# Performance work log

Measured on AMD Instinct MI355X. Metric: run time of the kernel, lower is better.

Reference implementation:

```python
import jax, jax.numpy as jnp
import numpy as np

N_VERTS = 200000
NNZ = 1600000
C_IN = 128
C_OUT = 128


def setup_inputs() -> dict:
    key = jax.random.key(0)
    k1, k2, k3, k4, k5, k6 = jax.random.split(key, 6)
    x = jax.random.normal(k1, (N_VERTS, C_IN), dtype=jnp.float32)
    rows = jax.random.randint(k2, (NNZ,), 0, N_VERTS, dtype=jnp.int64)
    cols = jax.random.randint(k3, (NNZ,), 0, N_VERTS, dtype=jnp.int64)
    vals = jax.random.normal(k4, (NNZ,), dtype=jnp.float32)
    W = jax.random.normal(k5, (C_OUT, C_IN), dtype=jnp.float32) * (1.0 / np.sqrt(C_IN))
    b = jax.random.normal(k6, (C_OUT,), dtype=jnp.float32) * 0.01
    return {"x": x, "rows": rows, "cols": cols, "vals": vals, "W": W, "b": b}


def reference(x, rows, cols, vals, W, b):
    # SpMM: out[r] += vals[e] * x[cols[e]]  (F = 2I - L in COO form)
    n = x.shape[0]
    agg = jax.ops.segment_sum(vals[:, None] * x[cols], rows, num_segments=n)  # [N, C_in]
    # Dense Linear projection: agg @ W^T + b
    return agg @ W.T + b  # [N, C_out]
```

## Files before the change

### kernel.cpp

```cpp
#include <hip/hip_runtime.h>

#define NV 200000
#define NE 1600000
#define CD 128
#define NBUCK 3125
#define NBLK 64
#define CHUNK 25600

#define Y_OFF      0UL
#define WB_OFF     51200000UL
#define CNT_OFF    51232768UL
#define TOT_OFF    52032768UL
#define START_OFF  52045312UL
#define SCAT_OFF   52058112UL
#define ROWOFF_OFF 64858112UL
#define SCAT2_OFF  65658368UL

typedef short  short8 __attribute__((ext_vector_type(8)));
typedef float  f32x4  __attribute__((ext_vector_type(4)));

__device__ __forceinline__ short bf16of(float f) {
    __bf16 h = (__bf16)f;
    return __builtin_bit_cast(short, h);
}

__global__ __launch_bounds__(256) void k_cvtW(const float* __restrict__ W,
                                              unsigned short* __restrict__ Wb) {
    int i = blockIdx.x * 256 + threadIdx.x;
    float4 wv = reinterpret_cast<const float4*>(W)[i];
    ushort4 o;
    o.x = (unsigned short)bf16of(wv.x);
    o.y = (unsigned short)bf16of(wv.y);
    o.z = (unsigned short)bf16of(wv.z);
    o.w = (unsigned short)bf16of(wv.w);
    reinterpret_cast<ushort4*>(Wb)[i] = o;
}

#define GEMM_BLOCKS 512
#define GEMM_WAVES (GEMM_BLOCKS * 4)
#define NTILES (NV / 16)

__global__ __launch_bounds__(256, 2) void gemm_mfma(const float* __restrict__ x,
                                                    const unsigned short* __restrict__ Wb,
                                                    unsigned short* __restrict__ y) {
    __shared__ __align__(16) short Wlds[2048 * 8];

    const int t = threadIdx.x;
    const int lane = t & 63;
    const int w = t >> 6;
    const int g = lane >> 4;

    {
        const uint4* Wg = reinterpret_cast<const uint4*>(Wb);
        uint4* L = reinterpret_cast<uint4*>(Wlds);
#pragma unroll
        for (int i = 0; i < 8; ++i) {
            int c = t + i * 256;
            int l = c & 63;
            int ks = (c >> 6) & 3;
            int tl = c >> 8;
            int row = 16 * tl + (l & 15);
            L[c] = Wg[row * 16 + ks * 4 + (l >> 4)];
        }
    }
    __syncthreads();

    short8 A[8][4];
    {
        const short8* L8 = reinterpret_cast<const short8*>(Wlds);
#pragma unroll
        for (int t8 = 0; t8 < 8; ++t8)
#pragma unroll
            for (int ks = 0; ks < 4; ++ks)
                A[t8][ks] = L8[(t8 * 4 + ks) * 64 + lane];
    }

    const int wgid = blockIdx.x * 4 + w;
    char* yb = reinterpret_cast<char*>(y);

    for (int tile = wgid; tile < NTILES; tile += GEMM_WAVES) {
        const int v0 = tile * 16;
        const int row = v0 + (lane & 15);
        const float4* xr = reinterpret_cast<const float4*>(x + (size_t)row * CD);

        float4 xf[8];
#pragma unroll
        for (int ks = 0; ks < 4; ++ks) {
            xf[2 * ks]     = xr[8 * ks + 2 * g];
            xf[2 * ks + 1] = xr[8 * ks + 2 * g + 1];
        }

        f32x4 acc[8];
#pragma unroll
        for (int t8 = 0; t8 < 8; ++t8) acc[t8] = (f32x4){0.f, 0.f, 0.f, 0.f};

#pragma unroll
        for (int ks = 0; ks < 4; ++ks) {
            short8 B;
            const float* f = reinterpret_cast<const float*>(&xf[2 * ks]);
#pragma unroll
            for (int j = 0; j < 8; ++j) B[j] = bf16of(f[j]);
#pragma unroll
            for (int t8 = 0; t8 < 8; ++t8)
                acc[t8] = __builtin_amdgcn_mfma_f32_16x16x32_bf16(A[t8][ks], B, acc[t8], 0, 0, 0);
        }

        const size_t rb = (size_t)(v0 + (lane & 15)) * 256;
#pragma unroll
        for (int t8 = 0; t8 < 8; ++t8) {
            ushort4 o;
            o.x = (unsigned short)bf16of(acc[t8][0]);
            o.y = (unsigned short)bf16of(acc[t8][1]);
            o.z = (unsigned short)bf16of(acc[t8][2]);
            o.w = (unsigned short)bf16of(acc[t8][3]);
            *reinterpret_cast<ushort4*>(yb + rb + t8 * 32 + g * 8) = o;
        }
    }
}

__global__ __launch_bounds__(1024) void pc(const int* __restrict__ rows,
                                           int* __restrict__ cnt) {
    __shared__ int hist[NBUCK];
    const int t = threadIdx.x;
    for (int i = t; i < NBUCK; i += 1024) hist[i] = 0;
    __syncthreads();
    const int e0 = blockIdx.x * CHUNK;
    const int e1 = min(NE, e0 + CHUNK);
    for (int e = e0 + t; e < e1; e += 1024)
        atomicAdd(&hist[rows[e] >> 6], 1);
    __syncthreads();
    for (int i = t; i < NBUCK; i += 1024)
        cnt[(size_t)blockIdx.x * NBUCK + i] = hist[i];
}

__global__ __launch_bounds__(256) void ps(int* __restrict__ cnt,
                                          int* __restrict__ tot) {
    int g = blockIdx.x * 256 + threadIdx.x;
    if (g >= NBUCK) return;
    int running = 0;
    for (int blk = 0; blk < NBLK; ++blk) {
        int idx = blk * NBUCK + g;
        int c = cnt[idx];
        cnt[idx] = running;
        running += c;
    }
    tot[g] = running;
}

__global__ __launch_bounds__(1024) void pt(const int* __restrict__ tot,
                                           int* __restrict__ start) {
    __shared__ int s[1024];
    const int t = threadIdx.x;
    if (t == 0) start[NBUCK] = NE;
    int carry = 0;
    for (int c = 0; c < 4; ++c) {
        int idx = c * 1024 + t;
        int v = (idx < NBUCK) ? tot[idx] : 0;
        s[t] = v;
        __syncthreads();
        for (int d = 1; d < 1024; d <<= 1) {
            int add = (t >= d) ? s[t - d] : 0;
            __syncthreads();
            s[t] += add;
            __syncthreads();
        }
        if (idx < NBUCK) start[idx] = carry + s[t] - v;
        carry += s[1023];
        __syncthreads();
    }
}

__global__ __launch_bounds__(1024) void px(const int* __restrict__ rows,
                                           const int* __restrict__ cols,
                                           const float* __restrict__ vals,
                                           const int* __restrict__ cnt,
                                           const int* __restrict__ start,
                                           int2* __restrict__ scat) {
    __shared__ int cur[NBUCK];
    const int t = threadIdx.x;
    for (int i = t; i < NBUCK; i += 1024)
        cur[i] = start[i] + cnt[(size_t)blockIdx.x * NBUCK + i];
    __syncthreads();
    const int e0 = blockIdx.x * CHUNK;
    const int e1 = min(NE, e0 + CHUNK);
    for (int e = e0 + t; e < e1; e += 1024) {
        int r = rows[e];
        int pos = atomicAdd(&cur[r >> 6], 1);
        scat[pos] = make_int2(cols[e] | ((r & 63) << 18), __float_as_int(vals[e]));
    }
}

__global__ __launch_bounds__(256) void k_sort(const int* __restrict__ start,
                                              const int2* __restrict__ scat,
                                              int2* __restrict__ scat2,
                                              int* __restrict__ rowoff) {
    __shared__ int rcnt[64], rinc[64], cur[64];
    const int t = threadIdx.x;
    const int b = blockIdx.x;
    const int s0 = start[b], s1 = start[b + 1];

    if (t < 64) rcnt[t] = 0;
    __syncthreads();
    for (int e = s0 + t; e < s1; e += 256)
        atomicAdd(&rcnt[(scat[e].x >> 18) & 63], 1);
    __syncthreads();
    if (t < 64) rinc[t] = rcnt[t];
    __syncthreads();
    for (int d = 1; d < 64; d <<= 1) {
        int add = 0;
        if (t < 64 && t >= d) add = rinc[t - d];
        __syncthreads();
        if (t < 64) rinc[t] += add;
        __syncthreads();
    }
    if (t < 64) {
        int excl = rinc[t] - rcnt[t];
        cur[t] = excl;
        rowoff[b * 64 + t] = s0 + excl;
    }
    if (b == NBUCK - 1 && t == 0) rowoff[NV] = NE;
    __syncthreads();
    for (int e = s0 + t; e < s1; e += 256) {
        int2 p = scat[e];
        int lr = (p.x >> 18) & 63;
        int pos = s0 + atomicAdd(&cur[lr], 1);
        scat2[pos] = p;
    }
}

#define BFLO(u) __uint_as_float((u) << 16)
#define BFHI(u) __uint_as_float((u) & 0xffff0000u)

__global__ __launch_bounds__(256) void k_gather(const int* __restrict__ rowoff,
                                                const int2* __restrict__ scat2,
                                                const unsigned* __restrict__ y,
                                                const float* __restrict__ b,
                                                float* __restrict__ out) {
    const int wid = threadIdx.x >> 6;
    const int lane = threadIdx.x & 63;
    const int half = lane >> 5;
    const int sl = lane & 31;
    const int row = blockIdx.x * 4 + wid;

    const int s0 = rowoff[row];
    const int n = rowoff[row + 1] - s0;
    const int nh = (n - half + 1) >> 1;

    float4 acc = half ? make_float4(0.f, 0.f, 0.f, 0.f)
                      : reinterpret_cast<const float4*>(b)[sl];
    const uint2* y2 = reinterpret_cast<const uint2*>(y);

    int k = 0;
    int e = s0 + half;
    for (; k + 4 <= nh; k += 4, e += 8) {
        int2 p0 = scat2[e];
        int2 p1 = scat2[e + 2];
        int2 p2 = scat2[e + 4];
        int2 p3 = scat2[e + 6];
        uint2 u0 = y2[(size_t)(p0.x & 0x3ffff) * 32 + sl];
        uint2 u1 = y2[(size_t)(p1.x & 0x3ffff) * 32 + sl];
        uint2 u2 = y2[(size_t)(p2.x & 0x3ffff) * 32 + sl];
        uint2 u3 = y2[(size_t)(p3.x & 0x3ffff) * 32 + sl];
        float v0 = __int_as_float(p0.y), v1 = __int_as_float(p1.y);
        float v2 = __int_as_float(p2.y), v3 = __int_as_float(p3.y);
        acc.x += (v0 * BFLO(u0.x) + v1 * BFLO(u1.x)) + (v2 * BFLO(u2.x) + v3 * BFLO(u3.x));
        acc.y += (v0 * BFHI(u0.x) + v1 * BFHI(u1.x)) + (v2 * BFHI(u2.x) + v3 * BFHI(u3.x));
        acc.z += (v0 * BFLO(u0.y) + v1 * BFLO(u1.y)) + (v2 * BFLO(u2.y) + v3 * BFLO(u3.y));
        acc.w += (v0 * BFHI(u0.y) + v1 * BFHI(u1.y)) + (v2 * BFHI(u2.y) + v3 * BFHI(u3.y));
    }
    for (; k < nh; ++k, e += 2) {
        int2 p = scat2[e];
        uint2 u = y2[(size_t)(p.x & 0x3ffff) * 32 + sl];
        float v = __int_as_float(p.y);
        acc.x += v * BFLO(u.x);
        acc.y += v * BFHI(u.x);
        acc.z += v * BFLO(u.y);
        acc.w += v * BFHI(u.y);
    }

    acc.x += __shfl_xor(acc.x, 32);
    acc.y += __shfl_xor(acc.y, 32);
    acc.z += __shfl_xor(acc.z, 32);
    acc.w += __shfl_xor(acc.w, 32);

    if (half == 0) {
        f32x4 st = {acc.x, acc.y, acc.z, acc.w};
        __builtin_nontemporal_store(st, (f32x4*)(out + (size_t)row * CD + sl * 4));
    }
}

extern "C" void kernel_launch(void* const* d_in, const int* in_sizes, int n_in,
                              void* d_out, int out_size, void* d_ws, size_t ws_size,
                              hipStream_t stream) {
    const float* x    = (const float*)d_in[0];
    const int*   rows = (const int*)d_in[1];
    const int*   cols = (const int*)d_in[2];
    const float* vals = (const float*)d_in[3];
    const float* Wm   = (const float*)d_in[4];
    const float* b    = (const float*)d_in[5];
    float* out = (float*)d_out;

    char* ws = (char*)d_ws;
    unsigned short* y  = (unsigned short*)(ws + Y_OFF);
    unsigned short* Wb = (unsigned short*)(ws + WB_OFF);
    int* cnt           = (int*)(ws + CNT_OFF);
    int* tot           = (int*)(ws + TOT_OFF);
    int* start         = (int*)(ws + START_OFF);
    int2* scat         = (int2*)(ws + SCAT_OFF);
    int* rowoff        = (int*)(ws + ROWOFF_OFF);
    int2* scat2        = (int2*)(ws + SCAT2_OFF);

    k_cvtW<<<16, 256, 0, stream>>>(Wm, Wb);
    gemm_mfma<<<GEMM_BLOCKS, 256, 0, stream>>>(x, Wb, y);
    pc<<<NBLK, 1024, 0, stream>>>(rows, cnt);
    ps<<<(NBUCK + 255) / 256, 256, 0, stream>>>(cnt, tot);
    pt<<<1, 1024, 0, stream>>>(tot, start);
    px<<<NBLK, 1024, 0, stream>>>(rows, cols, vals, cnt, start, scat);
    k_sort<<<NBUCK, 256, 0, stream>>>(start, scat, scat2, rowoff);
    k_gather<<<NV / 4, 256, 0, stream>>>(rowoff, scat2, (const unsigned*)y, b, out);
}
```

Measured before the change: 193.7 us.

## Fuse W conversion and row histogram into GEMM launch; widen gather loads

Removes the separate W-to-bf16 kernel by converting W to bf16 (round-to-nearest-even) inline while filling LDS in each GEMM block. It also merges the row-bucket histogram into the same launch as 64 extra blocks, so histogramming runs alongside the GEMM. The gather kernel now splits each wave into four 16-lane groups that each load full 16-byte bf16 rows, then reduces with two shuffles, replacing the two 32-lane halves doing 8-byte loads. This saves two launches and issues fewer, wider loads, at the cost of redundant W conversion in every GEMM block and histogram blocks running at 256 threads instead of 1024.

After: 184.1 us. 5.0% less time.

```diff
diff --git a/kernel.cpp b/kernel.cpp
--- a/kernel.cpp
+++ b/kernel.cpp
@@ -8,7 +8,6 @@
 #define CHUNK 25600
 
 #define Y_OFF      0UL
-#define WB_OFF     51200000UL
 #define CNT_OFF    51232768UL
 #define TOT_OFF    52032768UL
 #define START_OFF  52045312UL
@@ -19,39 +18,54 @@
 typedef short  short8 __attribute__((ext_vector_type(8)));
 typedef float  f32x4  __attribute__((ext_vector_type(4)));
 
+__device__ __forceinline__ unsigned bf16pair(float a, float b) {
+    unsigned ua = __float_as_uint(a);
+    unsigned ub = __float_as_uint(b);
+    ua += 0x7fffu + ((ua >> 16) & 1u);
+    ub += 0x7fffu + ((ub >> 16) & 1u);
+    return (ua >> 16) | (ub & 0xffff0000u);
+}
+
 __device__ __forceinline__ short bf16of(float f) {
     __bf16 h = (__bf16)f;
     return __builtin_bit_cast(short, h);
 }
 
-__global__ __launch_bounds__(256) void k_cvtW(const float* __restrict__ W,
-                                              unsigned short* __restrict__ Wb) {
-    int i = blockIdx.x * 256 + threadIdx.x;
-    float4 wv = reinterpret_cast<const float4*>(W)[i];
-    ushort4 o;
-    o.x = (unsigned short)bf16of(wv.x);
-    o.y = (unsigned short)bf16of(wv.y);
-    o.z = (unsigned short)bf16of(wv.z);
-    o.w = (unsigned short)bf16of(wv.w);
-    reinterpret_cast<ushort4*>(Wb)[i] = o;
-}
-
+#define PC_BLOCKS 64
 #define GEMM_BLOCKS 512
 #define GEMM_WAVES (GEMM_BLOCKS * 4)
 #define NTILES (NV / 16)
 
-__global__ __launch_bounds__(256, 2) void gemm_mfma(const float* __restrict__ x,
-                                                    const unsigned short* __restrict__ Wb,
-                                                    unsigned short* __restrict__ y) {
-    __shared__ __align__(16) short Wlds[2048 * 8];
-
+__global__ __launch_bounds__(256, 2) void gemm_pc(const float* __restrict__ x,
+                                                  const float* __restrict__ Wm,
+                                                  unsigned short* __restrict__ y,
+                                                  const int* __restrict__ rows,
+                                                  int* __restrict__ cnt) {
+    __shared__ __align__(16) char smem[32768];
     const int t = threadIdx.x;
+
+    if (blockIdx.x < PC_BLOCKS) {
+        int* hist = reinterpret_cast<int*>(smem);
+        const int blk = blockIdx.x;
+        for (int i = t; i < NBUCK; i += 256) hist[i] = 0;
+        __syncthreads();
+        const int e0 = blk * CHUNK;
+        const int e1 = min(NE, e0 + CHUNK);
+        for (int e = e0 + t; e < e1; e += 256)
+            atomicAdd(&hist[rows[e] >> 6], 1);
+        __syncthreads();
+        for (int i = t; i < NBUCK; i += 256)
+            cnt[(size_t)blk * NBUCK + i] = hist[i];
+        return;
+    }
+
+    short* Wlds = reinterpret_cast<short*>(smem);
     const int lane = t & 63;
     const int w = t >> 6;
     const int g = lane >> 4;
 
     {
-        const uint4* Wg = reinterpret_cast<const uint4*>(Wb);
+        const float4* Wf4 = reinterpret_cast<const float4*>(Wm);
         uint4* L = reinterpret_cast<uint4*>(Wlds);
 #pragma unroll
         for (int i = 0; i < 8; ++i) {
@@ -60,7 +74,15 @@
             int ks = (c >> 6) & 3;
             int tl = c >> 8;
             int row = 16 * tl + (l & 15);
-            L[c] = Wg[row * 16 + ks * 4 + (l >> 4)];
+            int j = ks * 4 + (l >> 4);
+            float4 wa = Wf4[row * 32 + j * 2];
+            float4 wb = Wf4[row * 32 + j * 2 + 1];
+            uint4 u;
+            u.x = bf16pair(wa.x, wa.y);
+            u.y = bf16pair(wa.z, wa.w);
+            u.z = bf16pair(wb.x, wb.y);
+            u.w = bf16pair(wb.z, wb.w);
+            L[c] = u;
         }
     }
     __syncthreads();
@@ -75,7 +97,7 @@
                 A[t8][ks] = L8[(t8 * 4 + ks) * 64 + lane];
     }
 
-    const int wgid = blockIdx.x * 4 + w;
+    const int wgid = (blockIdx.x - PC_BLOCKS) * 4 + w;
     char* yb = reinterpret_cast<char*>(y);
 
     for (int tile = wgid; tile < NTILES; tile += GEMM_WAVES) {
@@ -116,21 +138,6 @@
             *reinterpret_cast<ushort4*>(yb + rb + t8 * 32 + g * 8) = o;
         }
     }
-}
-
-__global__ __launch_bounds__(1024) void pc(const int* __restrict__ rows,
-                                           int* __restrict__ cnt) {
-    __shared__ int hist[NBUCK];
-    const int t = threadIdx.x;
-    for (int i = t; i < NBUCK; i += 1024) hist[i] = 0;
-    __syncthreads();
-    const int e0 = blockIdx.x * CHUNK;
-    const int e1 = min(NE, e0 + CHUNK);
-    for (int e = e0 + t; e < e1; e += 1024)
-        atomicAdd(&hist[rows[e] >> 6], 1);
-    __syncthreads();
-    for (int i = t; i < NBUCK; i += 1024)
-        cnt[(size_t)blockIdx.x * NBUCK + i] = hist[i];
 }
 
 __global__ __launch_bounds__(256) void ps(int* __restrict__ cnt,
@@ -233,59 +240,72 @@
 
 __global__ __launch_bounds__(256) void k_gather(const int* __restrict__ rowoff,
                                                 const int2* __restrict__ scat2,
-                                                const unsigned* __restrict__ y,
+                                                const uint4* __restrict__ y4,
                                                 const float* __restrict__ b,
                                                 float* __restrict__ out) {
     const int wid = threadIdx.x >> 6;
     const int lane = threadIdx.x & 63;
-    const int half = lane >> 5;
-    const int sl = lane & 31;
+    const int q = lane >> 4;
+    const int sl = lane & 15;
     const int row = blockIdx.x * 4 + wid;
 
     const int s0 = rowoff[row];
     const int n = rowoff[row + 1] - s0;
-    const int nh = (n - half + 1) >> 1;
-
-    float4 acc = half ? make_float4(0.f, 0.f, 0.f, 0.f)
-                      : reinterpret_cast<const float4*>(b)[sl];
-    const uint2* y2 = reinterpret_cast<const uint2*>(y);
-
-    int k = 0;
-    int e = s0 + half;
-    for (; k + 4 <= nh; k += 4, e += 8) {
-        int2 p0 = scat2[e];
-        int2 p1 = scat2[e + 2];
-        int2 p2 = scat2[e + 4];
-        int2 p3 = scat2[e + 6];
-        uint2 u0 = y2[(size_t)(p0.x & 0x3ffff) * 32 + sl];
-        uint2 u1 = y2[(size_t)(p1.x & 0x3ffff) * 32 + sl];
-        uint2 u2 = y2[(size_t)(p2.x & 0x3ffff) * 32 + sl];
-        uint2 u3 = y2[(size_t)(p3.x & 0x3ffff) * 32 + sl];
-        float v0 = __int_as_float(p0.y), v1 = __int_as_float(p1.y);
-        float v2 = __int_as_float(p2.y), v3 = __int_as_float(p3.y);
-        acc.x += (v0 * BFLO(u0.x) + v1 * BFLO(u1.x)) + (v2 * BFLO(u2.x) + v3 * BFLO(u3.x));
-        acc.y += (v0 * BFHI(u0.x) + v1 * BFHI(u1.x)) + (v2 * BFHI(u2.x) + v3 * BFHI(u3.x));
-        acc.z += (v0 * BFLO(u0.y) + v1 * BFLO(u1.y)) + (v2 * BFLO(u2.y) + v3 * BFLO(u3.y));
-        acc.w += (v0 * BFHI(u0.y) + v1 * BFHI(u1.y)) + (v2 * BFHI(u2.y) + v3 * BFHI(u3.y));
-    }
-    for (; k < nh; ++k, e += 2) {
-        int2 p = scat2[e];
-        uint2 u = y2[(size_t)(p.x & 0x3ffff) * 32 + sl];
+
+    float4 accA, accB;
+    if (q == 0) {
+        accA = reinterpret_cast<const float4*>(b)[2 * sl];
+        accB = reinterpret_cast<const float4*>(b)[2 * sl + 1];
+    } else {
+        accA = make_float4(0.f, 0.f, 0.f, 0.f);
+        accB = make_float4(0.f, 0.f, 0.f, 0.f);
+    }
+
+    int k = q;
+    for (; k + 4 < n; k += 8) {
+        int2 pa = scat2[s0 + k];
+        int2 pb = scat2[s0 + k + 4];
+        uint4 ua = y4[(size_t)(pa.x & 0x3ffff) * 16 + sl];
+        uint4 ub = y4[(size_t)(pb.x & 0x3ffff) * 16 + sl];
+        float va = __int_as_float(pa.y), vb = __int_as_float(pb.y);
+        accA.x += va * BFLO(ua.x) + vb * BFLO(ub.x);
+        accA.y += va * BFHI(ua.x) + vb * BFHI(ub.x);
+        accA.z += va * BFLO(ua.y) + vb * BFLO(ub.y);
+        accA.w += va * BFHI(ua.y) + vb * BFHI(ub.y);
+        accB.x += va * BFLO(ua.z) + vb * BFLO(ub.z);
+        accB.y += va * BFHI(ua.z) + vb * BFHI(ub.z);
+        accB.z += va * BFLO(ua.w) + vb * BFLO(ub.w);
+        accB.w += va * BFHI(ua.w) + vb * BFHI(ub.w);
+    }
+    if (k < n) {
+        int2 p = scat2[s0 + k];
+        uint4 u = y4[(size_t)(p.x & 0x3ffff) * 16 + sl];
         float v = __int_as_float(p.y);
-        acc.x += v * BFLO(u.x);
-        acc.y += v * BFHI(u.x);
-        acc.z += v * BFLO(u.y);
-        acc.w += v * BFHI(u.y);
-    }
-
-    acc.x += __shfl_xor(acc.x, 32);
-    acc.y += __shfl_xor(acc.y, 32);
-    acc.z += __shfl_xor(acc.z, 32);
-    acc.w += __shfl_xor(acc.w, 32);
-
-    if (half == 0) {
-        f32x4 st = {acc.x, acc.y, acc.z, acc.w};
-        __builtin_nontemporal_store(st, (f32x4*)(out + (size_t)row * CD + sl * 4));
+        accA.x += v * BFLO(u.x);
+        accA.y += v * BFHI(u.x);
+        accA.z += v * BFLO(u.y);
+        accA.w += v * BFHI(u.y);
+        accB.x += v * BFLO(u.z);
+        accB.y += v * BFHI(u.z);
+        accB.z += v * BFLO(u.w);
+        accB.w += v * BFHI(u.w);
+    }
+
+    accA.x += __shfl_xor(accA.x, 16); accA.x += __shfl_xor(accA.x, 32);
+    accA.y += __shfl_xor(accA.y, 16); accA.y += __shfl_xor(accA.y, 32);
+    accA.z += __shfl_xor(accA.z, 16); accA.z += __shfl_xor(accA.z, 32);
+    accA.w += __shfl_xor(accA.w, 16); accA.w += __shfl_xor(accA.w, 32);
+    accB.x += __shfl_xor(accB.x, 16); accB.x += __shfl_xor(accB.x, 32);
+    accB.y += __shfl_xor(accB.y, 16); accB.y += __shfl_xor(accB.y, 32);
+    accB.z += __shfl_xor(accB.z, 16); accB.z += __shfl_xor(accB.z, 32);
+    accB.w += __shfl_xor(accB.w, 16); accB.w += __shfl_xor(accB.w, 32);
+
+    if (q == 0) {
+        f32x4 sA = {accA.x, accA.y, accA.z, accA.w};
+        f32x4 sB = {accB.x, accB.y, accB.z, accB.w};
+        float* o = out + (size_t)row * CD + sl * 8;
+        __builtin_nontemporal_store(sA, (f32x4*)o);
+        __builtin_nontemporal_store(sB, (f32x4*)(o + 4));
     }
 }
 
@@ -302,7 +322,6 @@
 
     char* ws = (char*)d_ws;
     unsigned short* y  = (unsigned short*)(ws + Y_OFF);
-    unsigned short* Wb = (unsigned short*)(ws + WB_OFF);
     int* cnt           = (int*)(ws + CNT_OFF);
     int* tot           = (int*)(ws + TOT_OFF);
     int* start         = (int*)(ws + START_OFF);
@@ -310,12 +329,10 @@
     int* rowoff        = (int*)(ws + ROWOFF_OFF);
     int2* scat2        = (int2*)(ws + SCAT2_OFF);
 
-    k_cvtW<<<16, 256, 0, stream>>>(Wm, Wb);
-    gemm_mfma<<<GEMM_BLOCKS, 256, 0, stream>>>(x, Wb, y);
-    pc<<<NBLK, 1024, 0, stream>>>(rows, cnt);
+    gemm_pc<<<PC_BLOCKS + GEMM_BLOCKS, 256, 0, stream>>>(x, Wm, y, rows, cnt);
     ps<<<(NBUCK + 255) / 256, 256, 0, stream>>>(cnt, tot);
     pt<<<1, 1024, 0, stream>>>(tot, start);
     px<<<NBLK, 1024, 0, stream>>>(rows, cols, vals, cnt, start, scat);
     k_sort<<<NBUCK, 256, 0, stream>>>(start, scat, scat2, rowoff);
-    k_gather<<<NV / 4, 256, 0, stream>>>(rowoff, scat2, (const unsigned*)y, b, out);
-}
+    k_gather<<<NV / 4, 256, 0, stream>>>(rowoff, scat2, (const uint4*)y, b, out);
+}
```
